# Kernel optimization log

Hardware: AMD Instinct MI355X
Metric: run time of the kernel (lower is better)

Reference implementation:

```python
import jax, jax.numpy as jnp
import numpy as np

NUM_HEADS = 16
EPS = 1e-6
ROPE_BASE = 10000.0

def _thw(N, TT):
    table = {2640: (3, 22, 40), 1530: (3, 17, 30), 6120: (3, 34, 60), 660: (3, 11, 20)}
    return table.get(N - TT, (3, 23, 40))

def _positions(t, h, w):
    tt, hh, ww = np.meshgrid(np.arange(t), np.arange(h), np.arange(w), indexing='ij')
    return jnp.asarray(np.stack([tt, hh, ww], -1).reshape(-1, 3), jnp.float32)  # (THW, 3)

def _rope1d(x, pos):
    # x: (B,H,T,d) one axis-chunk, pos: (T,) positions for that axis
    d = x.shape[-1]
    inv_freq = 1.0 / (ROPE_BASE ** (jnp.arange(0, d, 2, dtype=jnp.float32) / d))
    ang = pos[:, None] * inv_freq                     # (T, d/2)
    cos = jnp.concatenate([jnp.cos(ang)] * 2, -1)     # (T, d)
    sin = jnp.concatenate([jnp.sin(ang)] * 2, -1)
    x1, x2 = x[..., : d // 2], x[..., d // 2:]
    return x * cos + jnp.concatenate([-x2, x1], -1) * sin

def _rope3d(x, pos, TT):
    # first TT tokens (text) pass through; video tokens get per-axis rotation
    pre, vid = x[:, :, :TT], x[:, :, TT:]
    chunks = jnp.split(vid, 3, axis=-1)               # t/h/w axis chunks
    rot = [_rope1d(c, pos[:, i]) for i, c in enumerate(chunks)]
    return jnp.concatenate([pre, jnp.concatenate(rot, -1)], axis=2)

def _rms(x, w):
    return x * jax.lax.rsqrt(jnp.mean(x * x, -1, keepdims=True) + EPS) * w

def setup_inputs() -> dict:
    key = jax.random.key(0)
    ks = jax.random.split(key, 12)
    B, N, C = 1, 2866, 1536
    Dh = C // NUM_HEADS
    s = 0.02
    return {
        'x': jax.random.normal(ks[0], (B, N, C), jnp.float32),
        'Wq': jax.random.normal(ks[1], (C, C), jnp.float32) * s,
        'bq': jnp.zeros((C,), jnp.float32),
        'Wk': jax.random.normal(ks[2], (C, C), jnp.float32) * s,
        'bk': jnp.zeros((C,), jnp.float32),
        'Wv': jax.random.normal(ks[3], (C, C), jnp.float32) * s,
        'bv': jnp.zeros((C,), jnp.float32),
        'qn_w': jnp.ones((Dh,), jnp.float32),
        'kn_w': jnp.ones((Dh,), jnp.float32),
        'Wp': jax.random.normal(ks[4], (C, C), jnp.float32) * s,
        'bp': jnp.zeros((C,), jnp.float32),
        'TT': 226,
    }

def reference(x, Wq, bq, Wk, bk, Wv, bv, qn_w, kn_w, Wp, bp, TT):
    B, N, C = x.shape
    H = NUM_HEADS
    Dh = C // H
    def proj(W, b):
        return (x @ W.T + b).reshape(B, N, H, Dh).transpose(0, 2, 1, 3)  # (B,H,N,Dh)
    q, k, v = proj(Wq, bq), proj(Wk, bk), proj(Wv, bv)
    q, k = _rms(q, qn_w), _rms(k, kn_w)
    t, h, w = _thw(N, TT)
    pos = _positions(t, h, w)
    q = _rope3d(q, pos, TT)
    k = _rope3d(k, pos, TT)
    scale = Dh ** -0.5
    attn = jax.nn.softmax(jnp.einsum('bhqd,bhkd->bhqk', q, k) * scale, axis=-1)
    o = jnp.einsum('bhqk,bhkd->bhqd', attn, v)
    o = o.transpose(0, 2, 1, 3).reshape(B, N, C)
    return o @ Wp.T + bp
```

## Files before the change

kernel.cpp:

```cpp
#include <hip/hip_runtime.h>
#include <hip/hip_bf16.h>
#include <math.h>

#define C_DIM 1536
#define H_NUM 16
#define DH    96

typedef __attribute__((ext_vector_type(4))) float  f32x4;
typedef __attribute__((ext_vector_type(8))) short  bf16x8;

__device__ __forceinline__ unsigned short f2bf_rne(float f) {
    unsigned u = __float_as_uint(f);
    unsigned r = (u + 0x7FFFu + ((u >> 16) & 1u)) >> 16;
    return (unsigned short)r;
}
__device__ __forceinline__ float bf2f(unsigned short h) {
    return __uint_as_float(((unsigned)h) << 16);
}

__device__ __forceinline__ void glds16(const void* g, void* l) {
    __builtin_amdgcn_global_load_lds(
        (const __attribute__((address_space(1))) unsigned int*)g,
        (__attribute__((address_space(3))) unsigned int*)l, 16, 0, 0);
}

__global__ __launch_bounds__(256)
void cvt_split(const float* __restrict__ in, unsigned short* __restrict__ hi,
               unsigned short* __restrict__ lo, int n4)
{
    const int i = blockIdx.x * 256 + threadIdx.x;
    if (i >= n4) return;
    float4 v = *(const float4*)&in[4 * i];
    unsigned short h[4], l[4];
    float vv[4] = {v.x, v.y, v.z, v.w};
    #pragma unroll
    for (int j = 0; j < 4; ++j) {
        h[j] = f2bf_rne(vv[j]);
        l[j] = f2bf_rne(vv[j] - bf2f(h[j]));
    }
    *(ushort4*)&hi[4 * i] = *(ushort4*)h;
    *(ushort4*)&lo[4 * i] = *(ushort4*)l;
}

struct CvtArgs {
    const float* src[4];
    unsigned short* hi[4];
    unsigned short* lo[4];
};
__global__ __launch_bounds__(256)
void cvt_split4(CvtArgs a, int n4)
{
    const int i = blockIdx.x * 256 + threadIdx.x;
    if (i >= n4) return;
    const int w = blockIdx.y;
    float4 v = *(const float4*)&a.src[w][4 * i];
    unsigned short h[4], l[4];
    float vv[4] = {v.x, v.y, v.z, v.w};
    #pragma unroll
    for (int j = 0; j < 4; ++j) {
        h[j] = f2bf_rne(vv[j]);
        l[j] = f2bf_rne(vv[j] - bf2f(h[j]));
    }
    *(ushort4*)&a.hi[w][4 * i] = *(ushort4*)h;
    *(ushort4*)&a.lo[w][4 * i] = *(ushort4*)l;
}

__global__ __launch_bounds__(256)
void gemm_mfma(const unsigned short* __restrict__ Ahi,
               const unsigned short* __restrict__ Alo,
               const unsigned short* W0h, const unsigned short* W0l,
               const float* b0, float* Y0,
               const unsigned short* W1h, const unsigned short* W1l,
               const float* b1, float* Y1,
               const unsigned short* W2h, const unsigned short* W2l,
               const float* b2, float* Y2,
               int M)
{
    __shared__ __align__(16) unsigned short lds[2 * 4 * 4096];

    const unsigned short* Wh;
    const unsigned short* Wl;
    const float* bias;
    float* Y;
    if (blockIdx.z == 0)      { Wh = W0h; Wl = W0l; bias = b0; Y = Y0; }
    else if (blockIdx.z == 1) { Wh = W1h; Wl = W1l; bias = b1; Y = Y1; }
    else                      { Wh = W2h; Wl = W2l; bias = b2; Y = Y2; }

    const int t   = threadIdx.x;
    const int m0  = blockIdx.x * 128;
    const int n0  = blockIdx.y * 128;
    const int w   = t >> 6;
    const int l   = t & 63;

    const unsigned short* src =
        (w == 0) ? Ahi : (w == 1) ? Alo : (w == 2) ? Wh : Wl;
    const int rbase = (w < 2) ? m0 : n0;
    const int rmax  = (w < 2) ? (M - 1) : 0x3FFFFFFF;
    const int srow  = l >> 2;
    const int scol  = l & 3;
    const int ssw   = (srow >> 1) & 3;
    int goff[8];
    #pragma unroll
    for (int i = 0; i < 8; ++i) {
        int gr = rbase + 16 * i + srow;
        gr = gr < rmax ? gr : rmax;
        goff[i] = gr * C_DIM + 8 * (scol ^ ssw);
    }

    const int lane = t & 63;
    const int wv   = t >> 6;
    const int wm   = wv & 1, wn = wv >> 1;
    const int lrow = lane & 15;
    const int quad = lane >> 4;
    const int pc   = quad ^ ((lrow >> 1) & 3);
    int aoff[4], boff[4];
    #pragma unroll
    for (int i = 0; i < 4; ++i) {
        aoff[i] = (64 * wm + 16 * i + lrow) * 32 + 8 * pc;
        boff[i] = (64 * wn + 16 * i + lrow) * 32 + 8 * pc;
    }

    f32x4 acc[4][4];
    #pragma unroll
    for (int i = 0; i < 4; ++i)
        #pragma unroll
        for (int j = 0; j < 4; ++j) acc[i][j] = (f32x4)0.f;

    #pragma unroll
    for (int i = 0; i < 8; ++i)
        glds16(src + goff[i], (char*)&lds[w * 4096] + i * 1024);

    const int NT = C_DIM / 32;
    for (int kt = 0; kt < NT; ++kt) {
        const int cb = kt & 1;
        const unsigned short* sA = lds + cb * 16384;

        asm volatile("s_waitcnt vmcnt(0)" ::: "memory");
        __builtin_amdgcn_s_barrier();
        __builtin_amdgcn_sched_barrier(0);

        bf16x8 ah[2], al[2], bh[4], bl[4];

        if (kt + 1 < NT) {
            char* dN = (char*)&lds[(cb ^ 1) * 16384 + w * 4096];
            const int k0n = (kt + 1) * 32;
            #pragma unroll
            for (int i = 0; i < 8; ++i)
                glds16(src + goff[i] + k0n, dN + i * 1024);
        }
        #pragma unroll
        for (int j = 0; j < 4; ++j) {
            bh[j] = *(const bf16x8*)&sA[8192 + boff[j]];
            bl[j] = *(const bf16x8*)&sA[12288 + boff[j]];
        }
        #pragma unroll
        for (int i = 0; i < 2; ++i) {
            ah[i] = *(const bf16x8*)&sA[aoff[i]];
            al[i] = *(const bf16x8*)&sA[4096 + aoff[i]];
        }
        __builtin_amdgcn_s_barrier();
        asm volatile("s_waitcnt lgkmcnt(0)" ::: "memory");
        __builtin_amdgcn_sched_barrier(0);
        __builtin_amdgcn_s_setprio(1);
        #pragma unroll
        for (int i = 0; i < 2; ++i)
            #pragma unroll
            for (int j = 0; j < 4; ++j) {
                acc[i][j] = __builtin_amdgcn_mfma_f32_16x16x32_bf16(ah[i], bh[j], acc[i][j], 0, 0, 0);
                acc[i][j] = __builtin_amdgcn_mfma_f32_16x16x32_bf16(al[i], bh[j], acc[i][j], 0, 0, 0);
                acc[i][j] = __builtin_amdgcn_mfma_f32_16x16x32_bf16(ah[i], bl[j], acc[i][j], 0, 0, 0);
            }
        __builtin_amdgcn_s_setprio(0);
        __builtin_amdgcn_s_barrier();
        __builtin_amdgcn_sched_barrier(0);

        #pragma unroll
        for (int i = 0; i < 2; ++i) {
            ah[i] = *(const bf16x8*)&sA[aoff[2 + i]];
            al[i] = *(const bf16x8*)&sA[4096 + aoff[2 + i]];
        }
        __builtin_amdgcn_s_barrier();
        asm volatile("s_waitcnt lgkmcnt(0)" ::: "memory");
        __builtin_amdgcn_sched_barrier(0);
        __builtin_amdgcn_s_setprio(1);
        #pragma unroll
        for (int i = 0; i < 2; ++i)
            #pragma unroll
            for (int j = 0; j < 4; ++j) {
                acc[2 + i][j] = __builtin_amdgcn_mfma_f32_16x16x32_bf16(ah[i], bh[j], acc[2 + i][j], 0, 0, 0);
                acc[2 + i][j] = __builtin_amdgcn_mfma_f32_16x16x32_bf16(al[i], bh[j], acc[2 + i][j], 0, 0, 0);
                acc[2 + i][j] = __builtin_amdgcn_mfma_f32_16x16x32_bf16(ah[i], bl[j], acc[2 + i][j], 0, 0, 0);
            }
        __builtin_amdgcn_s_setprio(0);
    }

    float bv[4];
    #pragma unroll
    for (int j = 0; j < 4; ++j) bv[j] = bias[n0 + 64 * wn + 16 * j + lrow];
    #pragma unroll
    for (int i = 0; i < 4; ++i) {
        const int rbase2 = m0 + 64 * wm + 16 * i + 4 * quad;
        #pragma unroll
        for (int p = 0; p < 4; ++p) {
            const int row = rbase2 + p;
            if (row >= M) continue;
            #pragma unroll
            for (int j = 0; j < 4; ++j) {
                const int col = n0 + 64 * wn + 16 * j + lrow;
                Y[(size_t)row * C_DIM + col] = acc[i][j][p] + bv[j];
            }
        }
    }
}

__global__ __launch_bounds__(512, 2)
void gemm_mfma256(const unsigned short* __restrict__ Ahi,
                  const unsigned short* __restrict__ Alo,
                  const unsigned short* W0h, const unsigned short* W0l,
                  const float* b0, float* Y0,
                  const unsigned short* W1h, const unsigned short* W1l,
                  const float* b1, float* Y1,
                  const unsigned short* W2h, const unsigned short* W2l,
                  const float* b2, float* Y2,
                  int M)
{
    extern __shared__ __align__(16) unsigned short smem[];

    const unsigned short* Wh;
    const unsigned short* Wl;
    const float* bias;
    float* Y;
    if (blockIdx.z == 0)      { Wh = W0h; Wl = W0l; bias = b0; Y = Y0; }
    else if (blockIdx.z == 1) { Wh = W1h; Wl = W1l; bias = b1; Y = Y1; }
    else                      { Wh = W2h; Wl = W2l; bias = b2; Y = Y2; }

    const int t    = threadIdx.x;
    const int wv   = t >> 6;
    const int lane = t & 63;
    const int m0   = blockIdx.x * 256;
    const int n0   = blockIdx.y * 256;

    const int mat  = wv >> 1;
    const int half = wv & 1;
    const unsigned short* src =
        (mat == 0) ? Ahi : (mat == 1) ? Alo : (mat == 2) ? Wh : Wl;
    const int rbase = (mat < 2) ? m0 : n0;
    const int rmax  = (mat < 2) ? (M - 1) : 0x3FFFFFFF;
    const int srow  = lane >> 2;
    const int scol  = lane & 3;
    const int ssw   = (srow >> 1) & 3;
    int goff[8];
    #pragma unroll
    for (int i = 0; i < 8; ++i) {
        int gr = rbase + half * 128 + 16 * i + srow;
        gr = gr < rmax ? gr : rmax;
        goff[i] = gr * C_DIM + 8 * (scol ^ ssw);
    }
    unsigned short* const dstBase = smem + mat * 8192 + half * 4096;

    const int wm   = wv & 1;
    const int wn   = wv >> 1;
    const int lrow = lane & 15;
    const int quad = lane >> 4;
    const int pc   = quad ^ ((lrow >> 1) & 3);
    int aoff[8], boff[4];
    #pragma unroll
    for (int i = 0; i < 8; ++i)
        aoff[i] = (128 * wm + 16 * i + lrow) * 32 + 8 * pc;
    #pragma unroll
    for (int j = 0; j < 4; ++j)
        boff[j] = (64 * wn + 16 * j + lrow) * 32 + 8 * pc;

    f32x4 acc[8][4];
    #pragma unroll
    for (int i = 0; i < 8; ++i)
        #pragma unroll
        for (int j = 0; j < 4; ++j) acc[i][j] = (f32x4)0.f;

    #pragma unroll
    for (int i = 0; i < 8; ++i)
        glds16(src + goff[i], (char*)dstBase + i * 1024);

    const int NT = C_DIM / 32;
    for (int kt = 0; kt < NT; ++kt) {
        const int cb = kt & 1;
        const unsigned short* sA = smem + cb * 32768;
        unsigned short* dN = dstBase + (cb ^ 1) * 32768;
        const int k0n = (kt + 1) * 32;
        const bool pf = (kt + 1 < NT);

        asm volatile("s_waitcnt vmcnt(0)" ::: "memory");
        __builtin_amdgcn_s_barrier();
        __builtin_amdgcn_sched_barrier(0);

        bf16x8 bh[4], bl[4], ah[2], al[2];

        if (pf) {
            #pragma unroll
            for (int i = 0; i < 8; ++i)
                glds16(src + goff[i] + k0n, (char*)dN + i * 1024);
        }
        #pragma unroll
        for (int j = 0; j < 4; ++j) {
            bh[j] = *(const bf16x8*)&sA[16384 + boff[j]];
            bl[j] = *(const bf16x8*)&sA[24576 + boff[j]];
        }
        #pragma unroll
        for (int i = 0; i < 2; ++i) {
            ah[i] = *(const bf16x8*)&sA[aoff[i]];
            al[i] = *(const bf16x8*)&sA[8192 + aoff[i]];
        }
        __builtin_amdgcn_s_barrier();
        asm volatile("s_waitcnt lgkmcnt(0)" ::: "memory");
        __builtin_amdgcn_sched_barrier(0);
        __builtin_amdgcn_s_setprio(1);
        #pragma unroll
        for (int i = 0; i < 2; ++i)
            #pragma unroll
            for (int j = 0; j < 4; ++j) {
                acc[i][j] = __builtin_amdgcn_mfma_f32_16x16x32_bf16(ah[i], bh[j], acc[i][j], 0, 0, 0);
                acc[i][j] = __builtin_amdgcn_mfma_f32_16x16x32_bf16(al[i], bh[j], acc[i][j], 0, 0, 0);
                acc[i][j] = __builtin_amdgcn_mfma_f32_16x16x32_bf16(ah[i], bl[j], acc[i][j], 0, 0, 0);
            }
        __builtin_amdgcn_s_setprio(0);
        __builtin_amdgcn_s_barrier();
        __builtin_amdgcn_sched_barrier(0);

        #pragma unroll
        for (int i = 0; i < 2; ++i) {
            ah[i] = *(const bf16x8*)&sA[aoff[2 + i]];
            al[i] = *(const bf16x8*)&sA[8192 + aoff[2 + i]];
        }
        __builtin_amdgcn_s_barrier();
        asm volatile("s_waitcnt lgkmcnt(0)" ::: "memory");
        __builtin_amdgcn_sched_barrier(0);
        __builtin_amdgcn_s_setprio(1);
        #pragma unroll
        for (int i = 0; i < 2; ++i)
            #pragma unroll
            for (int j = 0; j < 4; ++j) {
                acc[2 + i][j] = __builtin_amdgcn_mfma_f32_16x16x32_bf16(ah[i], bh[j], acc[2 + i][j], 0, 0, 0);
                acc[2 + i][j] = __builtin_amdgcn_mfma_f32_16x16x32_bf16(al[i], bh[j], acc[2 + i][j], 0, 0, 0);
                acc[2 + i][j] = __builtin_amdgcn_mfma_f32_16x16x32_bf16(ah[i], bl[j], acc[2 + i][j], 0, 0, 0);
            }
        __builtin_amdgcn_s_setprio(0);
        __builtin_amdgcn_s_barrier();
        __builtin_amdgcn_sched_barrier(0);

        #pragma unroll
        for (int i = 0; i < 2; ++i) {
            ah[i] = *(const bf16x8*)&sA[aoff[4 + i]];
            al[i] = *(const bf16x8*)&sA[8192 + aoff[4 + i]];
        }
        __builtin_amdgcn_s_barrier();
        asm volatile("s_waitcnt lgkmcnt(0)" ::: "memory");
        __builtin_amdgcn_sched_barrier(0);
        __builtin_amdgcn_s_setprio(1);
        #pragma unroll
        for (int i = 0; i < 2; ++i)
            #pragma unroll
            for (int j = 0; j < 4; ++j) {
                acc[4 + i][j] = __builtin_amdgcn_mfma_f32_16x16x32_bf16(ah[i], bh[j], acc[4 + i][j], 0, 0, 0);
                acc[4 + i][j] = __builtin_amdgcn_mfma_f32_16x16x32_bf16(al[i], bh[j], acc[4 + i][j], 0, 0, 0);
                acc[4 + i][j] = __builtin_amdgcn_mfma_f32_16x16x32_bf16(ah[i], bl[j], acc[4 + i][j], 0, 0, 0);
            }
        __builtin_amdgcn_s_setprio(0);
        __builtin_amdgcn_s_barrier();
        __builtin_amdgcn_sched_barrier(0);

        #pragma unroll
        for (int i = 0; i < 2; ++i) {
            ah[i] = *(const bf16x8*)&sA[aoff[6 + i]];
            al[i] = *(const bf16x8*)&sA[8192 + aoff[6 + i]];
        }
        __builtin_amdgcn_s_barrier();
        asm volatile("s_waitcnt lgkmcnt(0)" ::: "memory");
        __builtin_amdgcn_sched_barrier(0);
        __builtin_amdgcn_s_setprio(1);
        #pragma unroll
        for (int i = 0; i < 2; ++i)
            #pragma unroll
            for (int j = 0; j < 4; ++j) {
                acc[6 + i][j] = __builtin_amdgcn_mfma_f32_16x16x32_bf16(ah[i], bh[j], acc[6 + i][j], 0, 0, 0);
                acc[6 + i][j] = __builtin_amdgcn_mfma_f32_16x16x32_bf16(al[i], bh[j], acc[6 + i][j], 0, 0, 0);
                acc[6 + i][j] = __builtin_amdgcn_mfma_f32_16x16x32_bf16(ah[i], bl[j], acc[6 + i][j], 0, 0, 0);
            }
        __builtin_amdgcn_s_setprio(0);
    }

    float bv2[4];
    #pragma unroll
    for (int j = 0; j < 4; ++j) bv2[j] = bias[n0 + 64 * wn + 16 * j + lrow];
    #pragma unroll
    for (int i = 0; i < 8; ++i) {
        const int rbase2 = m0 + 128 * wm + 16 * i + 4 * quad;
        #pragma unroll
        for (int p = 0; p < 4; ++p) {
            const int row = rbase2 + p;
            if (row >= M) continue;
            #pragma unroll
            for (int j = 0; j < 4; ++j) {
                const int col = n0 + 64 * wn + 16 * j + lrow;
                Y[(size_t)row * C_DIM + col] = acc[i][j][p] + bv2[j];
            }
        }
    }
}

__global__ __launch_bounds__(256)
void rms_rope_split(const float* __restrict__ q, const float* __restrict__ k,
                    const float* __restrict__ qw, const float* __restrict__ kw,
                    const int* __restrict__ TTp,
                    unsigned short* __restrict__ qhi,
                    unsigned short* __restrict__ khi, int Ntok)
{
    const int idx = blockIdx.x * 256 + threadIdx.x;
    if (idx >= Ntok * H_NUM) return;
    const int h = idx & (H_NUM - 1);
    const int n = idx >> 4;

    const float* src;
    const float* w;
    if (blockIdx.y == 0) { src = q; w = qw; } else { src = k; w = kw; }
    const float* p = src + (size_t)n * C_DIM + h * DH;

    float x[DH];
    #pragma unroll
    for (int i = 0; i < DH / 4; ++i) *(float4*)&x[4 * i] = *(const float4*)&p[4 * i];

    float ss = 0.f;
    #pragma unroll
    for (int i = 0; i < DH; ++i) ss += x[i] * x[i];
    const float r = rsqrtf(ss * (1.0f / DH) + 1e-6f);
    #pragma unroll
    for (int i = 0; i < DH; ++i) x[i] *= r * w[i];

    const int TT = *TTp;
    if (n >= TT) {
        const int pidx = n - TT;
        const int NT = Ntok - TT;
        int hh = 23, ww = 40;
        if      (NT == 2640) { hh = 22; ww = 40; }
        else if (NT == 1530) { hh = 17; ww = 30; }
        else if (NT == 6120) { hh = 34; ww = 60; }
        else if (NT ==  660) { hh = 11; ww = 20; }
        float pos[3];
        pos[0] = (float)(pidx / (hh * ww));
        pos[1] = (float)((pidx / ww) % hh);
        pos[2] = (float)(pidx % ww);
        #pragma unroll
        for (int c = 0; c < 3; ++c) {
            #pragma unroll
            for (int j = 0; j < 16; ++j) {
                const float invf = exp2f(-0.83048202373f * (float)j);
                const float ang  = pos[c] * invf;
                const float cs = cosf(ang), sn = sinf(ang);
                const float a = x[32 * c + j], b = x[32 * c + j + 16];
                x[32 * c + j]      = a * cs - b * sn;
                x[32 * c + j + 16] = a * sn + b * cs;
            }
        }
    }

    const size_t off = (size_t)n * C_DIM + h * DH;
    const float qscale = 0.14724445f;
    if (blockIdx.y == 0) {
        #pragma unroll
        for (int i = 0; i < DH / 4; ++i) {
            unsigned short hb[4];
            #pragma unroll
            for (int j = 0; j < 4; ++j) hb[j] = f2bf_rne(x[4 * i + j] * qscale);
            *(ushort4*)&qhi[off + 4 * i] = *(ushort4*)hb;
        }
    } else {
        #pragma unroll
        for (int i = 0; i < DH / 4; ++i) {
            unsigned short hb[4];
            #pragma unroll
            for (int j = 0; j < 4; ++j) hb[j] = f2bf_rne(x[4 * i + j]);
            *(ushort4*)&khi[off + 4 * i] = *(ushort4*)hb;
        }
    }
}

__global__ __launch_bounds__(256)
void transpose_v(const float* __restrict__ V, unsigned short* __restrict__ vt,
                 int Ntok, int vtStride)
{
    __shared__ unsigned short tile[96 * 72];
    const int t  = threadIdx.x;
    const int k0 = blockIdx.x * 64;
    const int h  = blockIdx.y;

    #pragma unroll
    for (int it = 0; it < 6; ++it) {
        const int idx = t + 256 * it;
        const int key = idx / 24, dg = idx % 24;
        float vv[4] = {0.f, 0.f, 0.f, 0.f};
        if (k0 + key < Ntok)
            *(float4*)vv = *(const float4*)&V[(size_t)(k0 + key) * C_DIM + h * DH + 4 * dg];
        #pragma unroll
        for (int j = 0; j < 4; ++j) tile[(4 * dg + j) * 72 + key] = f2bf_rne(vv[j]);
    }
    __syncthreads();
    #pragma unroll
    for (int it = 0; it < 3; ++it) {
        const int idx = t + 256 * it;
        const int d = idx >> 3, ck = idx & 7;
        *(bf16x8*)&vt[((size_t)h * DH + d) * vtStride + k0 + 8 * ck] =
            *(const bf16x8*)&tile[d * 72 + 8 * ck];
    }
}

__global__ __launch_bounds__(256)
void attn_mfma(const unsigned short* __restrict__ qhi,
               const unsigned short* __restrict__ khi,
               const unsigned short* __restrict__ vt,
               unsigned short* __restrict__ Ohi,
               unsigned short* __restrict__ Olo,
               int Ntok, int nKt, int vtStride)
{
    __shared__ unsigned short ldsK[64 * 96];
    __shared__ unsigned short ldsV[96 * 72];
    __shared__ unsigned short ldsP[64 * 72];
    __shared__ float ldsL[64];

    const int t    = threadIdx.x;
    const int lane = t & 63;
    const int wv   = t >> 6;
    const int lrow = lane & 15;
    const int quad = lane >> 4;

    const int Lb  = blockIdx.x + gridDim.x * blockIdx.y;
    const int xcd = Lb & 7;
    const int jj  = Lb >> 3;
    const int h   = 2 * xcd + (jj >= nKt ? 1 : 0);
    const int q0  = (jj >= nKt ? jj - nKt : jj) * 64;
    const size_t hoff = (size_t)h * DH;

    bf16x8 qh[3];
    {
        const int qr = q0 + wv * 16 + lrow;
        if (qr < Ntok) {
            const size_t base = (size_t)qr * C_DIM + hoff + quad * 8;
            #pragma unroll
            for (int kc = 0; kc < 3; ++kc)
                qh[kc] = *(const bf16x8*)&qhi[base + 32 * kc];
        } else {
            const bf16x8 z = {0,0,0,0,0,0,0,0};
            #pragma unroll
            for (int kc = 0; kc < 3; ++kc) qh[kc] = z;
        }
    }

    const int rK  = t >> 2;
    const int cK  = t & 3;
    const int swK = (rK >> 1) & 3;
    const int swf = (lrow >> 1) & 3;
    const int vd  = t >> 3;
    const int vck = t & 7;

    float lsum = 0.f;
    f32x4 oacc[6];
    #pragma unroll
    for (int dt = 0; dt < 6; ++dt) oacc[dt] = (f32x4)0.f;

    const bf16x8 zv = {0,0,0,0,0,0,0,0};
    bf16x8 pk[3], pv[3];
    #pragma unroll
    for (int it = 0; it < 3; ++it) {
        pk[it] = (rK < Ntok) ? *(const bf16x8*)&khi[(size_t)rK * C_DIM + hoff + 8 * (cK + 4 * it)] : zv;
        pv[it] = *(const bf16x8*)&vt[(hoff + vd + 32 * it) * vtStride + 8 * vck];
    }

    const int pRow = (wv * 16 + lrow) * 72;
    for (int kt = 0; kt < nKt; ++kt) {
        const int k0 = kt * 64;
        __syncthreads();
        #pragma unroll
        for (int it = 0; it < 3; ++it) {
            *(bf16x8*)&ldsK[rK * 96 + 8 * (4 * it + (cK ^ swK))] = pk[it];
            *(bf16x8*)&ldsV[(vd + 32 * it) * 72 + 8 * vck]       = pv[it];
        }
        __syncthreads();

        if (kt + 1 < nKt) {
            const int kn = k0 + 64;
            #pragma unroll
            for (int it = 0; it < 3; ++it) {
                pk[it] = (kn + rK < Ntok) ? *(const bf16x8*)&khi[(size_t)(kn + rK) * C_DIM + hoff + 8 * (cK + 4 * it)] : zv;
                pv[it] = *(const bf16x8*)&vt[(hoff + vd + 32 * it) * vtStride + kn + 8 * vck];
            }
        }

        f32x4 sacc[4];
        #pragma unroll
        for (int mt = 0; mt < 4; ++mt) sacc[mt] = (f32x4)0.f;
        #pragma unroll
        for (int kc = 0; kc < 3; ++kc) {
            #pragma unroll
            for (int mt = 0; mt < 4; ++mt) {
                bf16x8 kb = *(const bf16x8*)&ldsK[(lrow + 16 * mt) * 96 + 8 * (4 * kc + (quad ^ swf))];
                sacc[mt] = __builtin_amdgcn_mfma_f32_16x16x32_bf16(kb, qh[kc], sacc[mt], 0, 0, 0);
            }
        }

        if (kt + 1 < nKt) {
            #pragma unroll
            for (int mt = 0; mt < 4; ++mt) {
                float e[4];
                #pragma unroll
                for (int p = 0; p < 4; ++p) e[p] = exp2f(sacc[mt][p]);
                lsum += (e[0] + e[1]) + (e[2] + e[3]);
                unsigned u0 = __float_as_uint(e[0]) + 0x8000u;
                unsigned u1 = __float_as_uint(e[1]) + 0x8000u;
                unsigned u2 = __float_as_uint(e[2]) + 0x8000u;
                unsigned u3 = __float_as_uint(e[3]) + 0x8000u;
                uint2 pr;
                pr.x = __builtin_amdgcn_perm(u1, u0, 0x07060302u);
                pr.y = __builtin_amdgcn_perm(u3, u2, 0x07060302u);
                *(uint2*)&ldsP[pRow + 16 * mt + 4 * quad] = pr;
            }
        } else {
            const int kq = k0 + 4 * quad;
            #pragma unroll
            for (int mt = 0; mt < 4; ++mt) {
                float e[4];
                #pragma unroll
                for (int p = 0; p < 4; ++p)
                    e[p] = (kq + 16 * mt + p < Ntok) ? exp2f(sacc[mt][p]) : 0.f;
                lsum += (e[0] + e[1]) + (e[2] + e[3]);
                unsigned u0 = __float_as_uint(e[0]) + 0x8000u;
                unsigned u1 = __float_as_uint(e[1]) + 0x8000u;
                unsigned u2 = __float_as_uint(e[2]) + 0x8000u;
                unsigned u3 = __float_as_uint(e[3]) + 0x8000u;
                uint2 pr;
                pr.x = __builtin_amdgcn_perm(u1, u0, 0x07060302u);
                pr.y = __builtin_amdgcn_perm(u3, u2, 0x07060302u);
                *(uint2*)&ldsP[pRow + 16 * mt + 4 * quad] = pr;
            }
        }

        #pragma unroll
        for (int kc2 = 0; kc2 < 2; ++kc2) {
            bf16x8 pa = *(const bf16x8*)&ldsP[pRow + 32 * kc2 + 8 * quad];
            #pragma unroll
            for (int dt = 0; dt < 6; ++dt) {
                bf16x8 vb = *(const bf16x8*)&ldsV[(16 * dt + lrow) * 72 + 32 * kc2 + 8 * quad];
                oacc[dt] = __builtin_amdgcn_mfma_f32_16x16x32_bf16(pa, vb, oacc[dt], 0, 0, 0);
            }
        }
    }

    lsum += __shfl_xor(lsum, 16, 64);
    lsum += __shfl_xor(lsum, 32, 64);
    ldsL[wv * 16 + lrow] = lsum;
    #pragma unroll
    for (int p = 0; p < 4; ++p) {
        const int row = q0 + wv * 16 + quad * 4 + p;
        if (row >= Ntok) continue;
        const float rl = 1.0f / ldsL[wv * 16 + quad * 4 + p];
        const size_t rbase = (size_t)row * C_DIM + hoff + lrow;
        #pragma unroll
        for (int dt = 0; dt < 6; ++dt) {
            const float o = oacc[dt][p] * rl;
            const unsigned short hb = f2bf_rne(o);
            Ohi[rbase + 16 * dt] = hb;
            Olo[rbase + 16 * dt] = f2bf_rne(o - bf2f(hb));
        }
    }
}

extern "C" void kernel_launch(void* const* d_in, const int* in_sizes, int n_in,
                              void* d_out, int out_size, void* d_ws, size_t ws_size,
                              hipStream_t stream)
{
    const float* x   = (const float*)d_in[0];
    const float* Wq  = (const float*)d_in[1];
    const float* bq  = (const float*)d_in[2];
    const float* Wk  = (const float*)d_in[3];
    const float* bk  = (const float*)d_in[4];
    const float* Wv  = (const float*)d_in[5];
    const float* bv  = (const float*)d_in[6];
    const float* qnw = (const float*)d_in[7];
    const float* knw = (const float*)d_in[8];
    const float* Wp  = (const float*)d_in[9];
    const float* bp  = (const float*)d_in[10];
    const int*   TTp = (const int*)d_in[11];

    const int Ntok = in_sizes[0] / C_DIM;
    const int nKt  = (Ntok + 63) / 64;
    const int vtStride = nKt * 64;
    const size_t NC = (size_t)Ntok * C_DIM;
    const size_t CC = (size_t)C_DIM * C_DIM;
    float* out = (float*)d_out;

    static bool s_attr = false;
    if (!s_attr) {
        hipFuncSetAttribute(reinterpret_cast<const void*>(gemm_mfma256),
                            hipFuncAttributeMaxDynamicSharedMemorySize, 131072);
        s_attr = true;
    }

    float*          kbuf = (float*)d_ws;
    float*          vbuf = kbuf + NC;
    unsigned short* xhi  = (unsigned short*)(vbuf + NC);
    unsigned short* xlo  = xhi + NC;
    unsigned short* wsp  = xlo + NC;
    unsigned short* wqh = wsp + 0 * CC, *wql = wsp + 1 * CC;
    unsigned short* wkh = wsp + 2 * CC, *wkl = wsp + 3 * CC;
    unsigned short* wvh = wsp + 4 * CC, *wvl = wsp + 5 * CC;
    unsigned short* wph = wsp + 6 * CC, *wpl = wsp + 7 * CC;
    unsigned short* qhib = wsp + 8 * CC;
    unsigned short* khib = qhib + NC;
    unsigned short* vtb  = khib + NC;
    float*          qbuf = out;
    unsigned short* ohi  = (unsigned short*)kbuf;
    unsigned short* olo  = ohi + NC;

    cvt_split<<<dim3((NC / 4 + 255) / 256), 256, 0, stream>>>(x, xhi, xlo, (int)(NC / 4));
    CvtArgs ca;
    ca.src[0] = Wq; ca.hi[0] = wqh; ca.lo[0] = wql;
    ca.src[1] = Wk; ca.hi[1] = wkh; ca.lo[1] = wkl;
    ca.src[2] = Wv; ca.hi[2] = wvh; ca.lo[2] = wvl;
    ca.src[3] = Wp; ca.hi[3] = wph; ca.lo[3] = wpl;
    cvt_split4<<<dim3((CC / 4 + 255) / 256, 4), 256, 0, stream>>>(ca, (int)(CC / 4));

    dim3 qkvgrid((Ntok + 255) / 256, C_DIM / 256, 3);
    gemm_mfma256<<<qkvgrid, 512, 131072, stream>>>(xhi, xlo,
        wqh, wql, bq, qbuf,
        wkh, wkl, bk, kbuf,
        wvh, wvl, bv, vbuf, Ntok);

    const int nv = Ntok * H_NUM;
    rms_rope_split<<<dim3((nv + 255) / 256, 2), 256, 0, stream>>>(
        qbuf, kbuf, qnw, knw, TTp, qhib, khib, Ntok);

    transpose_v<<<dim3(nKt, H_NUM), 256, 0, stream>>>(vbuf, vtb, Ntok, vtStride);

    attn_mfma<<<dim3(nKt, H_NUM), 256, 0, stream>>>(
        qhib, khib, vtb, ohi, olo, Ntok, nKt, vtStride);

    dim3 pgrid((Ntok + 127) / 128, C_DIM / 128, 1);
    gemm_mfma<<<pgrid, 256, 0, stream>>>(ohi, olo,
        wph, wpl, bp, out,
        wph, wpl, bp, out,
        wph, wpl, bp, out, Ntok);
}
```

Baseline: 485.4 us.

## Merge conversion launches, fuse rms/rope with V transpose, split GEMM prefetch

Merges the x and weight fp32-to-bf16 split conversions into one launch, and fuses the q/k RMS-norm+RoPE kernel with the V transpose kernel into a single launch using block-index role dispatch. The RMS/RoPE path now streams the input twice instead of holding all 96 values in registers, which lowers register pressure at the cost of a second read. In the projection GEMM, the prefetch of the next K tile is split into two halves issued across the two MFMA phases to spread memory traffic. Launch overhead drops by two kernels, but the merged convert grid launches many idle blocks for the smaller weight roles.

```diff
diff --git a/kernel.cpp b/kernel.cpp
--- a/kernel.cpp
+++ b/kernel.cpp
@@ -24,13 +24,19 @@
         (__attribute__((address_space(3))) unsigned int*)l, 16, 0, 0);
 }
 
+struct CvtAll {
+    const float* src[5];
+    unsigned short* hi[5];
+    unsigned short* lo[5];
+};
 __global__ __launch_bounds__(256)
-void cvt_split(const float* __restrict__ in, unsigned short* __restrict__ hi,
-               unsigned short* __restrict__ lo, int n4)
+void cvt_all(CvtAll a, int n4x, int n4w)
 {
-    const int i = blockIdx.x * 256 + threadIdx.x;
+    const int role = blockIdx.y;
+    const int n4   = (role == 0) ? n4x : n4w;
+    const int i    = blockIdx.x * 256 + threadIdx.x;
     if (i >= n4) return;
-    float4 v = *(const float4*)&in[4 * i];
+    float4 v = *(const float4*)&a.src[role][4 * i];
     unsigned short h[4], l[4];
     float vv[4] = {v.x, v.y, v.z, v.w};
     #pragma unroll
@@ -38,31 +44,8 @@
         h[j] = f2bf_rne(vv[j]);
         l[j] = f2bf_rne(vv[j] - bf2f(h[j]));
     }
-    *(ushort4*)&hi[4 * i] = *(ushort4*)h;
-    *(ushort4*)&lo[4 * i] = *(ushort4*)l;
-}
-
-struct CvtArgs {
-    const float* src[4];
-    unsigned short* hi[4];
-    unsigned short* lo[4];
-};
-__global__ __launch_bounds__(256)
-void cvt_split4(CvtArgs a, int n4)
-{
-    const int i = blockIdx.x * 256 + threadIdx.x;
-    if (i >= n4) return;
-    const int w = blockIdx.y;
-    float4 v = *(const float4*)&a.src[w][4 * i];
-    unsigned short h[4], l[4];
-    float vv[4] = {v.x, v.y, v.z, v.w};
-    #pragma unroll
-    for (int j = 0; j < 4; ++j) {
-        h[j] = f2bf_rne(vv[j]);
-        l[j] = f2bf_rne(vv[j] - bf2f(h[j]));
-    }
-    *(ushort4*)&a.hi[w][4 * i] = *(ushort4*)h;
-    *(ushort4*)&a.lo[w][4 * i] = *(ushort4*)l;
+    *(ushort4*)&a.hi[role][4 * i] = *(ushort4*)h;
+    *(ushort4*)&a.lo[role][4 * i] = *(ushort4*)l;
 }
 
 __global__ __launch_bounds__(256)
@@ -297,7 +280,7 @@
 
         if (pf) {
             #pragma unroll
-            for (int i = 0; i < 8; ++i)
+            for (int i = 0; i < 4; ++i)
                 glds16(src + goff[i] + k0n, (char*)dN + i * 1024);
         }
         #pragma unroll
@@ -326,6 +309,11 @@
         __builtin_amdgcn_s_barrier();
         __builtin_amdgcn_sched_barrier(0);
 
+        if (pf) {
+            #pragma unroll
+            for (int i = 4; i < 8; ++i)
+                glds16(src + goff[i] + k0n, (char*)dN + i * 1024);
+        }
         #pragma unroll
         for (int i = 0; i < 2; ++i) {
             ah[i] = *(const bf16x8*)&sA[aoff[2 + i]];
@@ -408,107 +396,139 @@
 }
 
 __global__ __launch_bounds__(256)
-void rms_rope_split(const float* __restrict__ q, const float* __restrict__ k,
-                    const float* __restrict__ qw, const float* __restrict__ kw,
-                    const int* __restrict__ TTp,
-                    unsigned short* __restrict__ qhi,
-                    unsigned short* __restrict__ khi, int Ntok)
-{
-    const int idx = blockIdx.x * 256 + threadIdx.x;
-    if (idx >= Ntok * H_NUM) return;
-    const int h = idx & (H_NUM - 1);
-    const int n = idx >> 4;
-
-    const float* src;
-    const float* w;
-    if (blockIdx.y == 0) { src = q; w = qw; } else { src = k; w = kw; }
-    const float* p = src + (size_t)n * C_DIM + h * DH;
-
-    float x[DH];
-    #pragma unroll
-    for (int i = 0; i < DH / 4; ++i) *(float4*)&x[4 * i] = *(const float4*)&p[4 * i];
-
-    float ss = 0.f;
-    #pragma unroll
-    for (int i = 0; i < DH; ++i) ss += x[i] * x[i];
-    const float r = rsqrtf(ss * (1.0f / DH) + 1e-6f);
-    #pragma unroll
-    for (int i = 0; i < DH; ++i) x[i] *= r * w[i];
-
-    const int TT = *TTp;
-    if (n >= TT) {
-        const int pidx = n - TT;
-        const int NT = Ntok - TT;
-        int hh = 23, ww = 40;
-        if      (NT == 2640) { hh = 22; ww = 40; }
-        else if (NT == 1530) { hh = 17; ww = 30; }
-        else if (NT == 6120) { hh = 34; ww = 60; }
-        else if (NT ==  660) { hh = 11; ww = 20; }
-        float pos[3];
-        pos[0] = (float)(pidx / (hh * ww));
-        pos[1] = (float)((pidx / ww) % hh);
-        pos[2] = (float)(pidx % ww);
-        #pragma unroll
-        for (int c = 0; c < 3; ++c) {
-            #pragma unroll
-            for (int j = 0; j < 16; ++j) {
-                const float invf = exp2f(-0.83048202373f * (float)j);
-                const float ang  = pos[c] * invf;
-                const float cs = cosf(ang), sn = sinf(ang);
-                const float a = x[32 * c + j], b = x[32 * c + j + 16];
-                x[32 * c + j]      = a * cs - b * sn;
-                x[32 * c + j + 16] = a * sn + b * cs;
-            }
-        }
-    }
-
-    const size_t off = (size_t)n * C_DIM + h * DH;
-    const float qscale = 0.14724445f;
-    if (blockIdx.y == 0) {
-        #pragma unroll
-        for (int i = 0; i < DH / 4; ++i) {
-            unsigned short hb[4];
-            #pragma unroll
-            for (int j = 0; j < 4; ++j) hb[j] = f2bf_rne(x[4 * i + j] * qscale);
-            *(ushort4*)&qhi[off + 4 * i] = *(ushort4*)hb;
-        }
-    } else {
-        #pragma unroll
-        for (int i = 0; i < DH / 4; ++i) {
-            unsigned short hb[4];
-            #pragma unroll
-            for (int j = 0; j < 4; ++j) hb[j] = f2bf_rne(x[4 * i + j]);
-            *(ushort4*)&khi[off + 4 * i] = *(ushort4*)hb;
-        }
-    }
-}
-
-__global__ __launch_bounds__(256)
-void transpose_v(const float* __restrict__ V, unsigned short* __restrict__ vt,
-                 int Ntok, int vtStride)
+void rms_rope_tv(const float* __restrict__ q, const float* __restrict__ k,
+                 const float* __restrict__ V,
+                 const float* __restrict__ qw, const float* __restrict__ kw,
+                 const int* __restrict__ TTp,
+                 unsigned short* __restrict__ qhi, unsigned short* __restrict__ khi,
+                 unsigned short* __restrict__ vt,
+                 int Ntok, int nKt, int vtStride)
 {
     __shared__ unsigned short tile[96 * 72];
-    const int t  = threadIdx.x;
-    const int k0 = blockIdx.x * 64;
-    const int h  = blockIdx.y;
-
-    #pragma unroll
-    for (int it = 0; it < 6; ++it) {
-        const int idx = t + 256 * it;
-        const int key = idx / 24, dg = idx % 24;
-        float vv[4] = {0.f, 0.f, 0.f, 0.f};
-        if (k0 + key < Ntok)
-            *(float4*)vv = *(const float4*)&V[(size_t)(k0 + key) * C_DIM + h * DH + 4 * dg];
-        #pragma unroll
-        for (int j = 0; j < 4; ++j) tile[(4 * dg + j) * 72 + key] = f2bf_rne(vv[j]);
-    }
-    __syncthreads();
-    #pragma unroll
-    for (int it = 0; it < 3; ++it) {
-        const int idx = t + 256 * it;
-        const int d = idx >> 3, ck = idx & 7;
-        *(bf16x8*)&vt[((size_t)h * DH + d) * vtStride + k0 + 8 * ck] =
-            *(const bf16x8*)&tile[d * 72 + 8 * ck];
+    const int halfB = (Ntok * H_NUM + 255) >> 8;
+
+    if ((int)blockIdx.x < 2 * halfB) {
+        const int role = blockIdx.x / halfB;
+        const int idx  = (blockIdx.x % halfB) * 256 + threadIdx.x;
+        if (idx >= Ntok * H_NUM) return;
+        const int h = idx & (H_NUM - 1);
+        const int n = idx >> 4;
+
+        const float* src = role == 0 ? q : k;
+        const float* w   = role == 0 ? qw : kw;
+        const float* p   = src + (size_t)n * C_DIM + h * DH;
+
+        float ss = 0.f;
+        #pragma unroll
+        for (int i = 0; i < DH / 4; ++i) {
+            float4 v4 = *(const float4*)&p[4 * i];
+            ss += v4.x * v4.x;
+            ss += v4.y * v4.y;
+            ss += v4.z * v4.z;
+            ss += v4.w * v4.w;
+        }
+        const float r = rsqrtf(ss * (1.0f / DH) + 1e-6f);
+
+        const int TT = *TTp;
+        const size_t off = (size_t)n * C_DIM + h * DH;
+        const float qscale = 0.14724445f;
+
+        if (n < TT) {
+            #pragma unroll
+            for (int i = 0; i < DH / 4; ++i) {
+                float4 v4 = *(const float4*)&p[4 * i];
+                float o[4] = {v4.x * (r * w[4 * i + 0]), v4.y * (r * w[4 * i + 1]),
+                              v4.z * (r * w[4 * i + 2]), v4.w * (r * w[4 * i + 3])};
+                unsigned short hb[4];
+                #pragma unroll
+                for (int j = 0; j < 4; ++j)
+                    hb[j] = (role == 0) ? f2bf_rne(o[j] * qscale) : f2bf_rne(o[j]);
+                if (role == 0) *(ushort4*)&qhi[off + 4 * i] = *(ushort4*)hb;
+                else           *(ushort4*)&khi[off + 4 * i] = *(ushort4*)hb;
+            }
+        } else {
+            const int pidx = n - TT;
+            const int NTt  = Ntok - TT;
+            int hh = 23, ww = 40;
+            if      (NTt == 2640) { hh = 22; ww = 40; }
+            else if (NTt == 1530) { hh = 17; ww = 30; }
+            else if (NTt == 6120) { hh = 34; ww = 60; }
+            else if (NTt ==  660) { hh = 11; ww = 20; }
+            float pos[3];
+            pos[0] = (float)(pidx / (hh * ww));
+            pos[1] = (float)((pidx / ww) % hh);
+            pos[2] = (float)(pidx % ww);
+            #pragma unroll
+            for (int c = 0; c < 3; ++c) {
+                float xa[16], xb[16];
+                #pragma unroll
+                for (int g = 0; g < 4; ++g) {
+                    float4 va = *(const float4*)&p[32 * c + 4 * g];
+                    float4 vb = *(const float4*)&p[32 * c + 16 + 4 * g];
+                    xa[4 * g + 0] = va.x * (r * w[32 * c + 4 * g + 0]);
+                    xa[4 * g + 1] = va.y * (r * w[32 * c + 4 * g + 1]);
+                    xa[4 * g + 2] = va.z * (r * w[32 * c + 4 * g + 2]);
+                    xa[4 * g + 3] = va.w * (r * w[32 * c + 4 * g + 3]);
+                    xb[4 * g + 0] = vb.x * (r * w[32 * c + 16 + 4 * g + 0]);
+                    xb[4 * g + 1] = vb.y * (r * w[32 * c + 16 + 4 * g + 1]);
+                    xb[4 * g + 2] = vb.z * (r * w[32 * c + 16 + 4 * g + 2]);
+                    xb[4 * g + 3] = vb.w * (r * w[32 * c + 16 + 4 * g + 3]);
+                }
+                #pragma unroll
+                for (int j = 0; j < 16; ++j) {
+                    const float invf = exp2f(-0.83048202373f * (float)j);
+                    const float ang  = pos[c] * invf;
+                    const float cs = cosf(ang), sn = sinf(ang);
+                    const float a = xa[j], b = xb[j];
+                    xa[j] = a * cs - b * sn;
+                    xb[j] = a * sn + b * cs;
+                }
+                #pragma unroll
+                for (int g = 0; g < 4; ++g) {
+                    unsigned short hb[4];
+                    #pragma unroll
+                    for (int j = 0; j < 4; ++j)
+                        hb[j] = (role == 0) ? f2bf_rne(xa[4 * g + j] * qscale)
+                                            : f2bf_rne(xa[4 * g + j]);
+                    if (role == 0) *(ushort4*)&qhi[off + 32 * c + 4 * g] = *(ushort4*)hb;
+                    else           *(ushort4*)&khi[off + 32 * c + 4 * g] = *(ushort4*)hb;
+                }
+                #pragma unroll
+                for (int g = 0; g < 4; ++g) {
+                    unsigned short hb[4];
+                    #pragma unroll
+                    for (int j = 0; j < 4; ++j)
+                        hb[j] = (role == 0) ? f2bf_rne(xb[4 * g + j] * qscale)
+                                            : f2bf_rne(xb[4 * g + j]);
+                    if (role == 0) *(ushort4*)&qhi[off + 32 * c + 16 + 4 * g] = *(ushort4*)hb;
+                    else           *(ushort4*)&khi[off + 32 * c + 16 + 4 * g] = *(ushort4*)hb;
+                }
+            }
+        }
+    } else {
+        const int b2 = blockIdx.x - 2 * halfB;
+        const int t  = threadIdx.x;
+        const int k0 = (b2 % nKt) * 64;
+        const int h  = b2 / nKt;
+
+        #pragma unroll
+        for (int it = 0; it < 6; ++it) {
+            const int idx = t + 256 * it;
+            const int key = idx / 24, dg = idx % 24;
+            float vv[4] = {0.f, 0.f, 0.f, 0.f};
+            if (k0 + key < Ntok)
+                *(float4*)vv = *(const float4*)&V[(size_t)(k0 + key) * C_DIM + h * DH + 4 * dg];
+            #pragma unroll
+            for (int j = 0; j < 4; ++j) tile[(4 * dg + j) * 72 + key] = f2bf_rne(vv[j]);
+        }
+        __syncthreads();
+        #pragma unroll
+        for (int it = 0; it < 3; ++it) {
+            const int idx = t + 256 * it;
+            const int d = idx >> 3, ck = idx & 7;
+            *(bf16x8*)&vt[((size_t)h * DH + d) * vtStride + k0 + 8 * ck] =
+                *(const bf16x8*)&tile[d * 72 + 8 * ck];
+        }
     }
 }
 
@@ -718,13 +738,14 @@
     unsigned short* ohi  = (unsigned short*)kbuf;
     unsigned short* olo  = ohi + NC;
 
-    cvt_split<<<dim3((NC / 4 + 255) / 256), 256, 0, stream>>>(x, xhi, xlo, (int)(NC / 4));
-    CvtArgs ca;
-    ca.src[0] = Wq; ca.hi[0] = wqh; ca.lo[0] = wql;
-    ca.src[1] = Wk; ca.hi[1] = wkh; ca.lo[1] = wkl;
-    ca.src[2] = Wv; ca.hi[2] = wvh; ca.lo[2] = wvl;
-    ca.src[3] = Wp; ca.hi[3] = wph; ca.lo[3] = wpl;
-    cvt_split4<<<dim3((CC / 4 + 255) / 256, 4), 256, 0, stream>>>(ca, (int)(CC / 4));
+    CvtAll ca;
+    ca.src[0] = x;  ca.hi[0] = xhi; ca.lo[0] = xlo;
+    ca.src[1] = Wq; ca.hi[1] = wqh; ca.lo[1] = wql;
+    ca.src[2] = Wk; ca.hi[2] = wkh; ca.lo[2] = wkl;
+    ca.src[3] = Wv; ca.hi[3] = wvh; ca.lo[3] = wvl;
+    ca.src[4] = Wp; ca.hi[4] = wph; ca.lo[4] = wpl;
+    cvt_all<<<dim3((NC / 4 + 255) / 256, 5), 256, 0, stream>>>(
+        ca, (int)(NC / 4), (int)(CC / 4));
 
     dim3 qkvgrid((Ntok + 255) / 256, C_DIM / 256, 3);
     gemm_mfma256<<<qkvgrid, 512, 131072, stream>>>(xhi, xlo,
@@ -732,11 +753,9 @@
         wkh, wkl, bk, kbuf,
         wvh, wvl, bv, vbuf, Ntok);
 
-    const int nv = Ntok * H_NUM;
-    rms_rope_split<<<dim3((nv + 255) / 256, 2), 256, 0, stream>>>(
-        qbuf, kbuf, qnw, knw, TTp, qhib, khib, Ntok);
-
-    transpose_v<<<dim3(nKt, H_NUM), 256, 0, stream>>>(vbuf, vtb, Ntok, vtStride);
+    const int halfB = (Ntok * H_NUM + 255) / 256;
+    rms_rope_tv<<<dim3(2 * halfB + nKt * H_NUM), 256, 0, stream>>>(
+        qbuf, kbuf, vbuf, qnw, knw, TTp, qhib, khib, vtb, Ntok, nKt, vtStride);
 
     attn_mfma<<<dim3(nKt, H_NUM), 256, 0, stream>>>(
         qhib, khib, vtb, ohi, olo, Ntok, nKt, vtStride);
```

Result: faster. 413.0 us (-14.9%).
